# Optimization experiments

Hardware: AMD Instinct MI355X
Metric: run time of the kernel (lower is better)

The kernel has to match this reference:

```python
import jax, jax.numpy as jnp
import numpy as np
import math

N_HEADS = 16
LN_EPS = 1e-5


def _layernorm(x, scale, bias):
    mu = jnp.mean(x, axis=-1, keepdims=True)
    var = jnp.var(x, axis=-1, keepdims=True)
    return (x - mu) * jax.lax.rsqrt(var + LN_EPS) * scale + bias


def _pos_encoding(seq_len, d_model, dtype):
    pos = jnp.arange(seq_len, dtype=jnp.float32)[:, None]
    div = jnp.exp(jnp.arange(0, d_model, 2, dtype=jnp.float32) * (-math.log(10000.0) / d_model))
    pe = jnp.zeros((seq_len, d_model), dtype=jnp.float32)
    pe = pe.at[:, 0::2].set(jnp.sin(pos * div))
    pe = pe.at[:, 1::2].set(jnp.cos(pos * div))
    return pe.astype(dtype)


def setup_inputs() -> dict:
    key = jax.random.key(0)
    ks = jax.random.split(key, 8)
    B, S, V, D, L = 2, 1024, 32000, 1024, 6
    F = 4 * D
    sc = 0.02
    return {
        "tokens": jax.random.randint(ks[0], (B, S), 0, V, dtype=jnp.int32),
        "token_emb": jax.random.normal(ks[1], (V, D), jnp.float32) * sc,
        "Wqkv": jax.random.normal(ks[2], (L, D, 3 * D), jnp.float32) * sc,
        "Wout": jax.random.normal(ks[3], (L, D, D), jnp.float32) * sc,
        "ln1_s": jnp.ones((L, D), jnp.float32),
        "ln1_b": jnp.zeros((L, D), jnp.float32),
        "W1": jax.random.normal(ks[4], (L, D, F), jnp.float32) * sc,
        "b1": jnp.zeros((L, F), jnp.float32),
        "W2": jax.random.normal(ks[5], (L, F, D), jnp.float32) * sc,
        "b2": jnp.zeros((L, D), jnp.float32),
        "ln2_s": jnp.ones((L, D), jnp.float32),
        "ln2_b": jnp.zeros((L, D), jnp.float32),
        "lnf_s": jnp.ones((D,), jnp.float32),
        "lnf_b": jnp.zeros((D,), jnp.float32),
        "Whead": jax.random.normal(ks[6], (D, V), jnp.float32) * sc,
        "bhead": jnp.zeros((V,), jnp.float32),
    }


def _forward(tokens, token_emb, Wqkv, Wout, ln1_s, ln1_b, W1, b1, W2, b2,
             ln2_s, ln2_b, lnf_s, lnf_b, Whead, bhead):
    B, S = tokens.shape
    D = token_emb.shape[1]
    L = Wqkv.shape[0]
    H = N_HEADS
    dk = D // H

    x = token_emb[tokens] + _pos_encoding(S, D, token_emb.dtype)  # [B,S,D]
    causal = jnp.tril(jnp.ones((S, S), dtype=bool))
    neg_inf = jnp.finfo(x.dtype).min

    for l in range(L):
        # --- attention sublayer ---
        h = _layernorm(x, ln1_s[l], ln1_b[l])
        qkv = (h @ Wqkv[l]).reshape(B, S, 3, H, dk)
        q, k, v = jnp.moveaxis(qkv, 2, 0)  # each [B,S,H,dk]
        scores = jnp.einsum('bqhd,bkhd->bhqk', q, k) / math.sqrt(dk)
        scores = jnp.where(causal, scores, neg_inf)
        attn = jax.nn.softmax(scores, axis=-1)  # [B,H,S,S]
        o = jnp.einsum('bhqk,bkhd->bqhd', attn, v).reshape(B, S, D)
        x = x + o @ Wout[l]
        # --- FFN sublayer ---
        h2 = _layernorm(x, ln2_s[l], ln2_b[l])
        x = x + jax.nn.gelu(h2 @ W1[l] + b1[l], approximate=False) @ W2[l] + b2[l]

    x = _layernorm(x, lnf_s, lnf_b)
    return x @ Whead + bhead  # [B,S,V]


def reference(tokens, token_emb, Wqkv, Wout, ln1_s, ln1_b, W1, b1, W2, b2,
              ln2_s, ln2_b, lnf_s, lnf_b, Whead, bhead):
    return _forward(tokens, token_emb, Wqkv, Wout, ln1_s, ln1_b, W1, b1, W2, b2,
                    ln2_s, ln2_b, lnf_s, lnf_b, Whead, bhead)
```

## Files before the change

kernel.cpp:

```cpp
#include <hip/hip_runtime.h>
#include <hip/hip_bf16.h>
#include <math.h>

typedef __bf16 bf16;
typedef __bf16 bf16x4 __attribute__((ext_vector_type(4)));
typedef __bf16 bf16x8 __attribute__((ext_vector_type(8)));
typedef float f32x4 __attribute__((ext_vector_type(4)));
typedef unsigned int u32x4 __attribute__((ext_vector_type(4)));

#define GL_AS(p) ((const __attribute__((address_space(1))) void*)(p))
#define LDS_AS(p) ((__attribute__((address_space(3))) void*)(p))

__device__ inline void xcd_remap(int& bm, int& bn, int NBM, int NBN)
{
    const int nwg = NBM * NBN;
    const int flat = bm + NBM * bn;
    const int q = nwg >> 3, r = nwg & 7;
    const int x = flat & 7, i = flat >> 3;
    const int f2 = ((x < r) ? x * (q + 1) : r * (q + 1) + (x - r) * q) + i;
    bm = f2 % NBM;
    bn = f2 / NBM;
}

struct TSeg {
    const float* in; bf16* out; int R, C, nTilesC, tilesPerZ, nTiles;
};

__global__ __launch_bounds__(256) void transpose_all_k(
    TSeg s0, TSeg s1, TSeg s2, TSeg s3, TSeg s4)
{
    int t = blockIdx.x;
    TSeg s;
    if (t < s0.nTiles) s = s0;
    else { t -= s0.nTiles;
    if (t < s1.nTiles) s = s1;
    else { t -= s1.nTiles;
    if (t < s2.nTiles) s = s2;
    else { t -= s2.nTiles;
    if (t < s3.nTiles) s = s3;
    else { t -= s3.nTiles; s = s4; }}}}

    const int z   = t / s.tilesPerZ;
    const int rem = t - z * s.tilesPerZ;
    const int cx  = rem % s.nTilesC, ry = rem / s.nTilesC;

    __shared__ float tl[32][33];
    const int c0 = cx * 32, r0 = ry * 32;
    const size_t zoff = (size_t)z * s.R * s.C;
    const float* inb = s.in + zoff;
    bf16* outb = s.out + zoff;
    const int tx = threadIdx.x, ty = threadIdx.y;
#pragma unroll
    for (int i = 0; i < 32; i += 8)
        tl[ty + i][tx] = inb[(size_t)(r0 + ty + i) * s.C + c0 + tx];
    __syncthreads();
#pragma unroll
    for (int i = 0; i < 32; i += 8)
        outb[(size_t)(c0 + ty + i) * s.R + r0 + tx] = (bf16)tl[tx][ty + i];
}

__global__ __launch_bounds__(256) void embed_k(
    const int* __restrict__ tok, const float* __restrict__ emb,
    float* __restrict__ x)
{
    const int D = 1024;
    const int row = blockIdx.x;
    const int s = row & 1023;
    const int t = tok[row];
    const int d0 = threadIdx.x * 4;
    const float c = 9.210340371976184f / 512.0f;
    const float div0 = expf(-(float)(d0 >> 1) * c);
    const float div1 = expf(-(float)((d0 >> 1) + 1) * c);
    const float a0 = (float)s * div0, a1 = (float)s * div1;
    const f32x4 e = *(const f32x4*)(emb + (size_t)t * D + d0);
    f32x4 o;
    o[0] = e[0] + sinf(a0);
    o[1] = e[1] + cosf(a0);
    o[2] = e[2] + sinf(a1);
    o[3] = e[3] + cosf(a1);
    *(f32x4*)(x + (size_t)row * D + d0) = o;
}

__global__ __launch_bounds__(256) void layernorm_k(
    const float* __restrict__ x, const float* __restrict__ sc,
    const float* __restrict__ bi, bf16* __restrict__ out)
{
    const int D = 1024;
    const int row = blockIdx.x;
    const int d0 = threadIdx.x * 4;
    const f32x4 v = *(const f32x4*)(x + (size_t)row * D + d0);
    float s = v[0] + v[1] + v[2] + v[3];
    float q = v[0] * v[0] + v[1] * v[1] + v[2] * v[2] + v[3] * v[3];
#pragma unroll
    for (int o = 32; o; o >>= 1) { s += __shfl_xor(s, o); q += __shfl_xor(q, o); }
    __shared__ float ls[4], lq[4];
    const int w = threadIdx.x >> 6;
    if ((threadIdx.x & 63) == 0) { ls[w] = s; lq[w] = q; }
    __syncthreads();
    const float S = ls[0] + ls[1] + ls[2] + ls[3];
    const float Q = lq[0] + lq[1] + lq[2] + lq[3];
    const float mu = S * (1.0f / D);
    const float var = Q * (1.0f / D) - mu * mu;
    const float rstd = rsqrtf(var + 1e-5f);
    const f32x4 sc4 = *(const f32x4*)(sc + d0);
    const f32x4 bi4 = *(const f32x4*)(bi + d0);
    bf16x4 o4;
#pragma unroll
    for (int i = 0; i < 4; ++i) o4[i] = (bf16)((v[i] - mu) * rstd * sc4[i] + bi4[i]);
    *(bf16x4*)(out + (size_t)row * D + d0) = o4;
}

template <int EPI, int SK = 1, bool SWZ = true>
__global__ __launch_bounds__(256, 2) void gemm_bt_k(
    const bf16* __restrict__ A, const bf16* __restrict__ Bt,
    float* __restrict__ Cf, bf16* __restrict__ Cb, bf16* __restrict__ Cb2,
    const float* __restrict__ bias, int M, int N, int K, int bn0)
{
    __shared__ __align__(16) bf16 Al[128 * 64];
    __shared__ __align__(16) bf16 Bl[128 * 64];
    const int tid = threadIdx.x;
    const int l = tid & 63;
    const int wbase = tid & 192;
    const int wr = (tid >> 7) & 1, wc = (tid >> 6) & 1;
    int bm = blockIdx.x, bn = blockIdx.y;
    if constexpr (SWZ) xcd_remap(bm, bn, gridDim.x, gridDim.y);
    const int kz = blockIdx.z;
    const int Kc = K / SK;

    f32x4 acc[4][4];
#pragma unroll
    for (int i = 0; i < 4; ++i)
#pragma unroll
        for (int j = 0; j < 4; ++j) acc[i][j] = (f32x4){0.f, 0.f, 0.f, 0.f};

    const bf16* Abase = A + (size_t)bm * 128 * K + (size_t)kz * Kc;
    const bf16* Bbase = Bt + (size_t)bn * 128 * K + (size_t)kz * Kc;

    for (int k0 = 0; k0 < Kc; k0 += 64) {
#pragma unroll
        for (int i = 0; i < 4; ++i) {
            const int c = i * 256 + tid;
            const int row = c >> 3, slot = c & 7;
            const int col = ((slot ^ (row & 7)) << 3);
            __builtin_amdgcn_global_load_lds(
                GL_AS(Abase + (size_t)row * K + k0 + col),
                LDS_AS(Al + (i * 256 + wbase) * 8), 16, 0, 0);
        }
#pragma unroll
        for (int i = 0; i < 4; ++i) {
            const int c = i * 256 + tid;
            const int row = c >> 3, slot = c & 7;
            const int col = ((slot ^ (row & 7)) << 3);
            __builtin_amdgcn_global_load_lds(
                GL_AS(Bbase + (size_t)row * K + k0 + col),
                LDS_AS(Bl + (i * 256 + wbase) * 8), 16, 0, 0);
        }
        __syncthreads();

#pragma unroll
        for (int ks = 0; ks < 2; ++ks) {
            bf16x8 af[4], bfr[4];
            const int kb = ks * 64 + ((l >> 4) << 4);
#pragma unroll
            for (int mi = 0; mi < 4; ++mi) {
                const int r = wr * 64 + mi * 16 + (l & 15);
                af[mi] = *(const bf16x8*)((const char*)Al + r * 128 + (kb ^ ((r & 7) << 4)));
            }
#pragma unroll
            for (int ni = 0; ni < 4; ++ni) {
                const int r = wc * 64 + ni * 16 + (l & 15);
                bfr[ni] = *(const bf16x8*)((const char*)Bl + r * 128 + (kb ^ ((r & 7) << 4)));
            }
#pragma unroll
            for (int mi = 0; mi < 4; ++mi)
#pragma unroll
                for (int ni = 0; ni < 4; ++ni)
                    acc[mi][ni] = __builtin_amdgcn_mfma_f32_16x16x32_bf16(
                        af[mi], bfr[ni], acc[mi][ni], 0, 0, 0);
        }
        __syncthreads();
    }

    const int colb = (bn0 + bn) * 128 + wc * 64;
    const int rowb = bm * 128 + wr * 64 + ((l >> 4) << 2);
#pragma unroll
    for (int mi = 0; mi < 4; ++mi) {
#pragma unroll
        for (int ni = 0; ni < 4; ++ni) {
            const int col = colb + ni * 16 + (l & 15);
            if constexpr (EPI == 5) {
                const int row0 = rowb + mi * 16;
                if (col < 2048) {
#pragma unroll
                    for (int j = 0; j < 4; ++j)
                        Cb[(size_t)(row0 + j) * N + col] = (bf16)acc[mi][ni][j];
                } else {
                    bf16x4 v4;
#pragma unroll
                    for (int j = 0; j < 4; ++j) v4[j] = (bf16)acc[mi][ni][j];
                    *(bf16x4*)&Cb2[((size_t)(row0 >> 3) * 1024 + (col - 2048)) * 8 + (row0 & 7)] = v4;
                }
            } else {
#pragma unroll
                for (int j = 0; j < 4; ++j) {
                    const int row = rowb + mi * 16 + j;
                    const float v = acc[mi][ni][j];
                    if constexpr (EPI == 0) {
                        Cb[(size_t)row * N + col] = (bf16)v;
                    } else if constexpr (EPI == 1) {
                        if constexpr (SK > 1) atomicAdd(&Cf[(size_t)row * N + col], v);
                        else                  Cf[(size_t)row * N + col] += v;
                    } else if constexpr (EPI == 2) {
                        const float u = v + bias[col];
                        const float g = 0.5f * u * (1.0f + erff(u * 0.70710678118654752f));
                        Cb[(size_t)row * N + col] = (bf16)g;
                    } else if constexpr (EPI == 3) {
                        const float add = (SK == 1 || kz == 0) ? v + bias[col] : v;
                        if constexpr (SK > 1) atomicAdd(&Cf[(size_t)row * N + col], add);
                        else                  Cf[(size_t)row * N + col] += add;
                    } else if constexpr (EPI == 4) {
                        Cf[(size_t)row * N + col] = v + bias[col];
                    }
                }
            }
        }
    }
}

__global__ __launch_bounds__(256) void attn_mfma_k(
    const bf16* __restrict__ qkv, const bf16* __restrict__ vt,
    bf16* __restrict__ o)
{
    __shared__ __align__(16) bf16 Kl[2][64 * 64];
    __shared__ __align__(16) bf16 Vl[2][64 * 64];
    __shared__ __align__(16) unsigned int Pp[4][16][76];

    const int tid = threadIdx.x;
    const int w = tid >> 6, l = tid & 63;
    const int g = l >> 4, lc = l & 15;
    const int bh = blockIdx.x >> 4;
    int qt = blockIdx.x & 15;
    if (bh & 16) qt = 15 - qt;
    const int h = bh & 15, b = bh >> 4;
    const int q0 = qt * 64;
    const int qw = q0 + w * 16;
    const int NT = qt + 1;

    const bf16* qbase = qkv + (size_t)b * 1024 * 3072 + h * 64;
    const bf16* kbase = qbase + 1024;
    const bf16* vbase = vt + (size_t)b * 128 * 8192 + h * 512;

    bf16x8 af0, af1;
    {
        const bf16* qp = qbase + (size_t)(qw + lc) * 3072 + g * 8;
        af0 = *(const bf16x8*)qp;
        af1 = *(const bf16x8*)(qp + 32);
    }

    f32x4 acc[4];
#pragma unroll
    for (int dt = 0; dt < 4; ++dt) acc[dt] = (f32x4){0.f, 0.f, 0.f, 0.f};
    f32x4 m  = (f32x4){-1e30f, -1e30f, -1e30f, -1e30f};
    f32x4 ls = (f32x4){0.f, 0.f, 0.f, 0.f};

    auto stage = [&](int t) {
        const int k0 = t * 64;
        const int buf = t & 1;
#pragma unroll
        for (int ld = 0; ld < 2; ++ld) {
            const int c = ld * 256 + tid;
            const int row = c >> 3;
            const int d = (((c & 7) ^ (row & 7)) << 3);
            __builtin_amdgcn_global_load_lds(
                GL_AS(kbase + (size_t)(k0 + row) * 3072 + d),
                LDS_AS(Kl[buf] + (ld * 256 + (tid & 192)) * 8), 16, 0, 0);
        }
#pragma unroll
        for (int ld = 0; ld < 2; ++ld) {
            const int c = ld * 256 + tid;
            const int row = c >> 3;
            const int so = (c & 7) ^ (row & 7);
            __builtin_amdgcn_global_load_lds(
                GL_AS(vbase + (size_t)((k0 >> 3) + so) * 8192 + row * 8),
                LDS_AS(Vl[buf] + (ld * 256 + (tid & 192)) * 8), 16, 0, 0);
        }
    };

    const float SCL = 0.18033688011112042f;

    auto compute = [&](int t, bool MASKED) {
        const char* KT = (const char*)Kl[t & 1];
        const char* VT = (const char*)Vl[t & 1];
        const int k0 = t * 64;

        f32x4 s[4];
#pragma unroll
        for (int kt = 0; kt < 4; ++kt) {
            const int r = kt * 16 + lc;
            const bf16x8 kf0 = *(const bf16x8*)(KT + r * 128 + ((g * 16)      ^ ((r & 7) << 4)));
            const bf16x8 kf1 = *(const bf16x8*)(KT + r * 128 + ((64 + g * 16) ^ ((r & 7) << 4)));
            f32x4 sv = (f32x4){0.f, 0.f, 0.f, 0.f};
            sv = __builtin_amdgcn_mfma_f32_16x16x32_bf16(af0, kf0, sv, 0, 0, 0);
            sv = __builtin_amdgcn_mfma_f32_16x16x32_bf16(af1, kf1, sv, 0, 0, 0);
            s[kt] = sv;
        }

#pragma unroll
        for (int kt = 0; kt < 4; ++kt)
#pragma unroll
            for (int j = 0; j < 4; ++j) {
                if (MASKED) {
                    const int row = qw + 4 * g + j;
                    s[kt][j] = (k0 + kt * 16 + lc <= row) ? s[kt][j] * SCL : -1e30f;
                } else {
                    s[kt][j] *= SCL;
                }
            }

        f32x4 tm;
#pragma unroll
        for (int j = 0; j < 4; ++j)
            tm[j] = fmaxf(fmaxf(s[0][j], s[1][j]), fmaxf(s[2][j], s[3][j]));
#pragma unroll
        for (int off = 8; off; off >>= 1)
#pragma unroll
            for (int j = 0; j < 4; ++j) tm[j] = fmaxf(tm[j], __shfl_xor(tm[j], off));

        f32x4 sc;
#pragma unroll
        for (int j = 0; j < 4; ++j) {
            const float mn = fmaxf(m[j], tm[j]);
            sc[j] = exp2f(m[j] - mn);
            m[j] = mn;
        }
        f32x4 p[4];
#pragma unroll
        for (int kt = 0; kt < 4; ++kt)
#pragma unroll
            for (int j = 0; j < 4; ++j) p[kt][j] = exp2f(s[kt][j] - m[j]);
#pragma unroll
        for (int j = 0; j < 4; ++j)
            ls[j] = ls[j] * sc[j] + ((p[0][j] + p[1][j]) + (p[2][j] + p[3][j]));
#pragma unroll
        for (int dt = 0; dt < 4; ++dt)
#pragma unroll
            for (int j = 0; j < 4; ++j) acc[dt][j] *= sc[j];

#pragma unroll
        for (int j = 0; j < 4; ++j) {
            const int r = 4 * g + j;
#pragma unroll
            for (int kt = 0; kt < 4; ++kt) {
                const bf16 hb = (bf16)p[kt][j];
                const bf16 lb = (bf16)(p[kt][j] - (float)hb);
                Pp[w][r][kt * 16 + lc] =
                    (unsigned)__builtin_bit_cast(unsigned short, hb) |
                    ((unsigned)__builtin_bit_cast(unsigned short, lb) << 16);
            }
        }
        bf16x8 pah[2], pal[2];
#pragma unroll
        for (int ks = 0; ks < 2; ++ks) {
            const unsigned* prow = &Pp[w][lc][ks * 32 + g * 8];
            const u32x4 ca = *(const u32x4*)prow;
            const u32x4 cb = *(const u32x4*)(prow + 4);
            u32x4 hh, ll;
            hh[0] = (ca[0] & 0xffffu) | (ca[1] << 16);
            hh[1] = (ca[2] & 0xffffu) | (ca[3] << 16);
            hh[2] = (cb[0] & 0xffffu) | (cb[1] << 16);
            hh[3] = (cb[2] & 0xffffu) | (cb[3] << 16);
            ll[0] = (ca[0] >> 16) | (ca[1] & 0xffff0000u);
            ll[1] = (ca[2] >> 16) | (ca[3] & 0xffff0000u);
            ll[2] = (cb[0] >> 16) | (cb[1] & 0xffff0000u);
            ll[3] = (cb[2] >> 16) | (cb[3] & 0xffff0000u);
            pah[ks] = __builtin_bit_cast(bf16x8, hh);
            pal[ks] = __builtin_bit_cast(bf16x8, ll);
        }

#pragma unroll
        for (int dt = 0; dt < 4; ++dt) {
            const int r = dt * 16 + lc;
            const bf16x8 vf0 = *(const bf16x8*)(VT + r * 128 + ((g * 16)      ^ ((r & 7) << 4)));
            const bf16x8 vf1 = *(const bf16x8*)(VT + r * 128 + ((64 + g * 16) ^ ((r & 7) << 4)));
            f32x4 a = acc[dt];
            a = __builtin_amdgcn_mfma_f32_16x16x32_bf16(pah[0], vf0, a, 0, 0, 0);
            a = __builtin_amdgcn_mfma_f32_16x16x32_bf16(pah[1], vf1, a, 0, 0, 0);
            a = __builtin_amdgcn_mfma_f32_16x16x32_bf16(pal[0], vf0, a, 0, 0, 0);
            a = __builtin_amdgcn_mfma_f32_16x16x32_bf16(pal[1], vf1, a, 0, 0, 0);
            acc[dt] = a;
        }
    };

    stage(0);
    __syncthreads();
    for (int t = 0; t < NT; ++t) {
        if (t + 1 < NT) stage(t + 1);
        compute(t, t == NT - 1);
        __syncthreads();
    }

    f32x4 inv;
#pragma unroll
    for (int j = 0; j < 4; ++j) {
        float s = ls[j];
#pragma unroll
        for (int off = 8; off; off >>= 1) s += __shfl_xor(s, off);
        inv[j] = 1.0f / s;
    }
    bf16* op = o + (size_t)(b * 1024 + qw) * 1024 + h * 64;
#pragma unroll
    for (int dt = 0; dt < 4; ++dt)
#pragma unroll
        for (int j = 0; j < 4; ++j)
            op[(size_t)(4 * g + j) * 1024 + dt * 16 + lc] = (bf16)(acc[dt][j] * inv[j]);
}

extern "C" void kernel_launch(void* const* d_in, const int* in_sizes, int n_in,
                              void* d_out, int out_size, void* d_ws, size_t ws_size,
                              hipStream_t stream)
{
    const int B = 2, S = 1024, D = 1024, L = 6, F = 4096, V = 32000, H = 16;
    const int M = B * S;

    const int*   tokens    = (const int*)  d_in[0];
    const float* token_emb = (const float*)d_in[1];
    const float* Wqkv      = (const float*)d_in[2];
    const float* Wout      = (const float*)d_in[3];
    const float* ln1_s     = (const float*)d_in[4];
    const float* ln1_b     = (const float*)d_in[5];
    const float* W1        = (const float*)d_in[6];
    const float* b1        = (const float*)d_in[7];
    const float* W2        = (const float*)d_in[8];
    const float* b2        = (const float*)d_in[9];
    const float* ln2_s     = (const float*)d_in[10];
    const float* ln2_b     = (const float*)d_in[11];
    const float* lnf_s     = (const float*)d_in[12];
    const float* lnf_b     = (const float*)d_in[13];
    const float* Whead     = (const float*)d_in[14];
    const float* bhead     = (const float*)d_in[15];
    float* out = (float*)d_out;

    char* w = (char*)d_ws;
    size_t off = 0;
    auto alloc = [&](size_t n) { char* p = w + off; off += (n + 255) & ~(size_t)255; return p; };
    bf16* WqkvT  = (bf16*)alloc((size_t)L * 3 * D * D * 2);
    bf16* WoutT  = (bf16*)alloc((size_t)L * D * D * 2);
    bf16* W1T    = (bf16*)alloc((size_t)L * F * D * 2);
    bf16* W2T    = (bf16*)alloc((size_t)L * D * F * 2);
    bf16* WheadT = (bf16*)alloc((size_t)V * D * 2);
    float* x     = (float*)alloc((size_t)M * D * 4);
    bf16* h      = (bf16*)alloc((size_t)M * D * 2);
    bf16* qkv    = (bf16*)alloc((size_t)M * 3 * D * 2);
    bf16* ob     = (bf16*)alloc((size_t)M * D * 2);
    bf16* mid    = (bf16*)alloc((size_t)M * F * 2);
    bf16* vt     = mid;

    TSeg s0{Wqkv,  WqkvT,  D, 3 * D, 3 * D / 32, (3 * D / 32) * (D / 32), (3 * D / 32) * (D / 32) * L};
    TSeg s1{Wout,  WoutT,  D, D,     D / 32,     (D / 32) * (D / 32),     (D / 32) * (D / 32) * L};
    TSeg s2{W1,    W1T,    D, F,     F / 32,     (F / 32) * (D / 32),     (F / 32) * (D / 32) * L};
    TSeg s3{W2,    W2T,    F, D,     D / 32,     (D / 32) * (F / 32),     (D / 32) * (F / 32) * L};
    TSeg s4{Whead, WheadT, D, V,     V / 32,     (V / 32) * (D / 32),     (V / 32) * (D / 32)};
    const int totTiles = s0.nTiles + s1.nTiles + s2.nTiles + s3.nTiles + s4.nTiles;
    transpose_all_k<<<totTiles, dim3(32, 8), 0, stream>>>(s0, s1, s2, s3, s4);

    embed_k<<<M, 256, 0, stream>>>(tokens, token_emb, x);

    for (int lyr = 0; lyr < L; ++lyr) {
        layernorm_k<<<M, 256, 0, stream>>>(x, ln1_s + lyr * D, ln1_b + lyr * D, h);
        gemm_bt_k<5><<<dim3(M / 128, 3 * D / 128), 256, 0, stream>>>(
            h, WqkvT + (size_t)lyr * 3 * D * D, nullptr, qkv, vt, nullptr, M, 3 * D, D, 0);
        attn_mfma_k<<<B * H * S / 64, 256, 0, stream>>>(qkv, vt, ob);
        gemm_bt_k<1, 2><<<dim3(M / 128, D / 128, 2), 256, 0, stream>>>(
            ob, WoutT + (size_t)lyr * D * D, x, nullptr, nullptr, nullptr, M, D, D, 0);
        layernorm_k<<<M, 256, 0, stream>>>(x, ln2_s + lyr * D, ln2_b + lyr * D, h);
        gemm_bt_k<2><<<dim3(M / 128, F / 128), 256, 0, stream>>>(
            h, W1T + (size_t)lyr * F * D, nullptr, mid, nullptr, b1 + lyr * F, M, F, D, 0);
        gemm_bt_k<3, 2><<<dim3(M / 128, D / 128, 2), 256, 0, stream>>>(
            mid, W2T + (size_t)lyr * D * F, x, nullptr, nullptr, b2 + lyr * D, M, D, F, 0);
    }
    layernorm_k<<<M, 256, 0, stream>>>(x, lnf_s, lnf_b, h);
    {
        const int slice[4] = {63, 63, 62, 62};
        int n0 = 0;
        for (int si = 0; si < 4; ++si) {
            gemm_bt_k<4, 1, false><<<dim3(M / 128, slice[si]), 256, 0, stream>>>(
                h, WheadT + (size_t)n0 * 128 * D, out, nullptr, nullptr, bhead,
                M, V, D, n0);
            n0 += slice[si];
        }
    }
}
```

Before: 1.509 ms.

## Vectorize weight transpose with 64x64 bf16 tiles and merge head GEMM launches

The weight transpose kernel now handles 64x64 tiles, reading float4 and converting to bf16 before storing into shared memory. It then writes bf16x4 vectors, cutting instruction count and using wider memory accesses. The vocab-head GEMM goes from four column-sliced launches to one full-grid launch, and the bn0 offset parameter is dropped. This saves launch overhead but may change cache behaviour for the large output write, and the bf16 shared-memory tile may see more bank conflicts on the column reads.

```diff
diff --git a/kernel.cpp b/kernel.cpp
--- a/kernel.cpp
+++ b/kernel.cpp
@@ -44,19 +44,31 @@
     const int rem = t - z * s.tilesPerZ;
     const int cx  = rem % s.nTilesC, ry = rem / s.nTilesC;
 
-    __shared__ float tl[32][33];
-    const int c0 = cx * 32, r0 = ry * 32;
+    __shared__ __align__(16) bf16 tl[64][66];
+    const int c0 = cx * 64, r0 = ry * 64;
     const size_t zoff = (size_t)z * s.R * s.C;
     const float* inb = s.in + zoff;
     bf16* outb = s.out + zoff;
-    const int tx = threadIdx.x, ty = threadIdx.y;
-#pragma unroll
-    for (int i = 0; i < 32; i += 8)
-        tl[ty + i][tx] = inb[(size_t)(r0 + ty + i) * s.C + c0 + tx];
+    const int tid = threadIdx.x;
+    const int q = tid & 15, p = tid >> 4;
+#pragma unroll
+    for (int i = 0; i < 4; ++i) {
+        const int r = p + i * 16;
+        const f32x4 v = *(const f32x4*)(inb + (size_t)(r0 + r) * s.C + c0 + q * 4);
+        bf16x4 b4;
+#pragma unroll
+        for (int k = 0; k < 4; ++k) b4[k] = (bf16)v[k];
+        *(bf16x4*)&tl[r][q * 4] = b4;
+    }
     __syncthreads();
 #pragma unroll
-    for (int i = 0; i < 32; i += 8)
-        outb[(size_t)(c0 + ty + i) * s.R + r0 + tx] = (bf16)tl[tx][ty + i];
+    for (int i = 0; i < 4; ++i) {
+        const int c = p + i * 16;
+        bf16x4 b4;
+#pragma unroll
+        for (int k = 0; k < 4; ++k) b4[k] = tl[q * 4 + k][c];
+        *(bf16x4*)&outb[(size_t)(c0 + c) * s.R + r0 + q * 4] = b4;
+    }
 }
 
 __global__ __launch_bounds__(256) void embed_k(
@@ -114,7 +126,7 @@
 __global__ __launch_bounds__(256, 2) void gemm_bt_k(
     const bf16* __restrict__ A, const bf16* __restrict__ Bt,
     float* __restrict__ Cf, bf16* __restrict__ Cb, bf16* __restrict__ Cb2,
-    const float* __restrict__ bias, int M, int N, int K, int bn0)
+    const float* __restrict__ bias, int M, int N, int K)
 {
     __shared__ __align__(16) bf16 Al[128 * 64];
     __shared__ __align__(16) bf16 Bl[128 * 64];
@@ -181,7 +193,7 @@
         __syncthreads();
     }
 
-    const int colb = (bn0 + bn) * 128 + wc * 64;
+    const int colb = bn * 128 + wc * 64;
     const int rowb = bm * 128 + wr * 64 + ((l >> 4) << 2);
 #pragma unroll
     for (int mi = 0; mi < 4; ++mi) {
@@ -455,38 +467,30 @@
     bf16* mid    = (bf16*)alloc((size_t)M * F * 2);
     bf16* vt     = mid;
 
-    TSeg s0{Wqkv,  WqkvT,  D, 3 * D, 3 * D / 32, (3 * D / 32) * (D / 32), (3 * D / 32) * (D / 32) * L};
-    TSeg s1{Wout,  WoutT,  D, D,     D / 32,     (D / 32) * (D / 32),     (D / 32) * (D / 32) * L};
-    TSeg s2{W1,    W1T,    D, F,     F / 32,     (F / 32) * (D / 32),     (F / 32) * (D / 32) * L};
-    TSeg s3{W2,    W2T,    F, D,     D / 32,     (D / 32) * (F / 32),     (D / 32) * (F / 32) * L};
-    TSeg s4{Whead, WheadT, D, V,     V / 32,     (V / 32) * (D / 32),     (V / 32) * (D / 32)};
+    TSeg s0{Wqkv,  WqkvT,  D, 3 * D, 3 * D / 64, (3 * D / 64) * (D / 64), (3 * D / 64) * (D / 64) * L};
+    TSeg s1{Wout,  WoutT,  D, D,     D / 64,     (D / 64) * (D / 64),     (D / 64) * (D / 64) * L};
+    TSeg s2{W1,    W1T,    D, F,     F / 64,     (F / 64) * (D / 64),     (F / 64) * (D / 64) * L};
+    TSeg s3{W2,    W2T,    F, D,     D / 64,     (D / 64) * (F / 64),     (D / 64) * (F / 64) * L};
+    TSeg s4{Whead, WheadT, D, V,     V / 64,     (V / 64) * (D / 64),     (V / 64) * (D / 64)};
     const int totTiles = s0.nTiles + s1.nTiles + s2.nTiles + s3.nTiles + s4.nTiles;
-    transpose_all_k<<<totTiles, dim3(32, 8), 0, stream>>>(s0, s1, s2, s3, s4);
+    transpose_all_k<<<totTiles, 256, 0, stream>>>(s0, s1, s2, s3, s4);
 
     embed_k<<<M, 256, 0, stream>>>(tokens, token_emb, x);
 
     for (int lyr = 0; lyr < L; ++lyr) {
         layernorm_k<<<M, 256, 0, stream>>>(x, ln1_s + lyr * D, ln1_b + lyr * D, h);
         gemm_bt_k<5><<<dim3(M / 128, 3 * D / 128), 256, 0, stream>>>(
-            h, WqkvT + (size_t)lyr * 3 * D * D, nullptr, qkv, vt, nullptr, M, 3 * D, D, 0);
+            h, WqkvT + (size_t)lyr * 3 * D * D, nullptr, qkv, vt, nullptr, M, 3 * D, D);
         attn_mfma_k<<<B * H * S / 64, 256, 0, stream>>>(qkv, vt, ob);
         gemm_bt_k<1, 2><<<dim3(M / 128, D / 128, 2), 256, 0, stream>>>(
-            ob, WoutT + (size_t)lyr * D * D, x, nullptr, nullptr, nullptr, M, D, D, 0);
+            ob, WoutT + (size_t)lyr * D * D, x, nullptr, nullptr, nullptr, M, D, D);
         layernorm_k<<<M, 256, 0, stream>>>(x, ln2_s + lyr * D, ln2_b + lyr * D, h);
         gemm_bt_k<2><<<dim3(M / 128, F / 128), 256, 0, stream>>>(
-            h, W1T + (size_t)lyr * F * D, nullptr, mid, nullptr, b1 + lyr * F, M, F, D, 0);
+            h, W1T + (size_t)lyr * F * D, nullptr, mid, nullptr, b1 + lyr * F, M, F, D);
         gemm_bt_k<3, 2><<<dim3(M / 128, D / 128, 2), 256, 0, stream>>>(
-            mid, W2T + (size_t)lyr * D * F, x, nullptr, nullptr, b2 + lyr * D, M, D, F, 0);
+            mid, W2T + (size_t)lyr * D * F, x, nullptr, nullptr, b2 + lyr * D, M, D, F);
     }
     layernorm_k<<<M, 256, 0, stream>>>(x, lnf_s, lnf_b, h);
-    {
-        const int slice[4] = {63, 63, 62, 62};
-        int n0 = 0;
-        for (int si = 0; si < 4; ++si) {
-            gemm_bt_k<4, 1, false><<<dim3(M / 128, slice[si]), 256, 0, stream>>>(
-                h, WheadT + (size_t)n0 * 128 * D, out, nullptr, nullptr, bhead,
-                M, V, D, n0);
-            n0 += slice[si];
-        }
-    }
-}
+    gemm_bt_k<4, 1, false><<<dim3(M / 128, V / 128), 256, 0, stream>>>(
+        h, WheadT, out, nullptr, nullptr, bhead, M, V, D);
+}
```

Result: faster. 1.474 ms (-2.3%).
